# Performance work log

Hardware: AMD Instinct MI355X
Metric: run time of the kernel (lower is better)

Reference implementation:

```python
import jax, jax.numpy as jnp
import numpy as np

N_NODES = 100000
N_EDGES = 1000000
HIDDEN = 128
GROUPS = [[0, 1, 2], [3, 4, 5], [6, 7, 8]]  # model_ids[i]['volume_ids']
COMBOS = [(0, 0), (0, 1), (0, 2), (1, 1), (1, 2), (2, 2)]  # combinations with replacement
LN_EPS = 1e-5


def _ln(h, g, b):
    m = jnp.mean(h, axis=-1, keepdims=True)
    v = jnp.var(h, axis=-1, keepdims=True)
    return (h - m) * jax.lax.rsqrt(v + LN_EPS) * g + b


def setup_inputs() -> dict:
    key = jax.random.key(0)
    ks = jax.random.split(key, 8)
    C = len(COMBOS)
    s = 0.02
    x = jax.random.normal(ks[0], (N_NODES, HIDDEN), jnp.float32)
    e = jax.random.normal(ks[1], (N_EDGES, HIDDEN), jnp.float32)
    edge_index = jax.random.randint(ks[2], (2, N_EDGES), 0, N_NODES)
    volume_id = jax.random.randint(ks[3], (N_NODES,), 0, 9)
    W1 = (jax.random.normal(ks[4], (C, 3 * HIDDEN, HIDDEN), jnp.float32) * s)
    b1 = jnp.zeros((C, HIDDEN), jnp.float32)
    g1 = jnp.ones((C, HIDDEN), jnp.float32)
    be1 = jnp.zeros((C, HIDDEN), jnp.float32)
    W2 = (jax.random.normal(ks[5], (C, HIDDEN, HIDDEN), jnp.float32) * s)
    b2 = jnp.zeros((C, HIDDEN), jnp.float32)
    g2 = jnp.ones((C, HIDDEN), jnp.float32)
    be2 = jnp.zeros((C, HIDDEN), jnp.float32)
    W3 = (jax.random.normal(ks[6], (C, HIDDEN, 1), jnp.float32) * s)
    b3 = jnp.zeros((C, 1), jnp.float32)
    return dict(x=x, edge_index=edge_index, e=e, volume_id=volume_id,
                W1=W1, b1=b1, g1=g1, be1=be1,
                W2=W2, b2=b2, g2=g2, be2=be2,
                W3=W3, b3=b3)


def reference(x, edge_index, e, volume_id, W1, b1, g1, be1, W2, b2, g2, be2, W3, b3):
    # volume id -> group id lookup (constant, from hparams['model_ids'])
    group_of_vol = np.zeros(9, dtype=np.int32)
    for gi, vols in enumerate(GROUPS):
        group_of_vol[vols] = gi
    group_of_vol = jnp.asarray(group_of_vol)

    start, end = edge_index[0], edge_index[1]
    gs = group_of_vol[volume_id[start]]  # [E] group of start node
    ge = group_of_vol[volume_id[end]]    # [E] group of end node
    xs = x[start]                        # [E, H] gather
    xe = x[end]                          # [E, H] gather

    out = jnp.zeros((start.shape[0], 1), x.dtype)
    for c, (ga, gb) in enumerate(COMBOS):
        mask = (gs == ga) & (ge == gb)   # torch.isin on disjoint volume groups
        # split first Linear to avoid materializing concat([xs, xe, e])
        h = xs @ W1[c, :HIDDEN] + xe @ W1[c, HIDDEN:2 * HIDDEN] + e @ W1[c, 2 * HIDDEN:] + b1[c]
        h = jax.nn.relu(_ln(h, g1[c], be1[c]))
        h = jax.nn.relu(_ln(h @ W2[c] + b2[c], g2[c], be2[c]))
        logit = h @ W3[c] + b3[c]        # [E, 1]
        out = jnp.where(mask[:, None], logit, out)  # masked scatter into shared buffer
    return out
```

## Files before the change

### kernel.cpp

```cpp
#include <hip/hip_runtime.h>

#define E_EDGES 1000000
#define N_NODES 100000
#define HID 128

static constexpr int    WS_CMB  = 256;
static constexpr int    WS_LIST = 1000448;
static constexpr int    WS_W1F  = 5001984;
static constexpr int    WS_W2F  = 5591808;

typedef __bf16 bf16x8 __attribute__((ext_vector_type(8)));
typedef float  f32x4  __attribute__((ext_vector_type(4)));

__device__ __forceinline__ unsigned short f2bf(float f) {
    unsigned int u = __builtin_bit_cast(unsigned int, f);
    u = (u + 0x7FFFu + ((u >> 16) & 1u)) >> 16;
    return (unsigned short)u;
}

__global__ void k_wconv(const float* __restrict__ W1, const float* __restrict__ W2,
                        unsigned short* __restrict__ w1f, unsigned short* __restrict__ w2f) {
    int idx = blockIdx.x * 256 + threadIdx.x;
    if (idx < 294912) {
        int j = idx & 7, lane = (idx >> 3) & 63, nt = (idx >> 9) & 7;
        int t = idx >> 12;
        int c = t / 12, kt = t - c * 12;
        int k = kt * 32 + ((lane >> 4) << 3) + j;
        int n = (nt << 4) + (lane & 15);
        w1f[idx] = f2bf(W1[(c * 384 + k) * 128 + n]);
    } else {
        int i2 = idx - 294912;
        int j = i2 & 7, lane = (i2 >> 3) & 63, nt = (i2 >> 9) & 7;
        int t = i2 >> 12;
        int c = t >> 2, kt = t & 3;
        int k = kt * 32 + ((lane >> 4) << 3) + j;
        int n = (nt << 4) + (lane & 15);
        w2f[i2] = f2bf(W2[(c * 128 + k) * 128 + n]);
    }
}

__global__ void k_classify(const int* __restrict__ ei, const int* __restrict__ vol,
                           signed char* __restrict__ cmb, float* __restrict__ out,
                           int* __restrict__ counts) {
    __shared__ int bc[6];
    int tid = threadIdx.x;
    if (tid < 6) bc[tid] = 0;
    __syncthreads();
    int eid = blockIdx.x * 256 + tid;
    if (eid < E_EDGES) {
        int s = ei[eid], t = ei[E_EDGES + eid];
        int gs = vol[s] / 3, ge = vol[t] / 3;
        int cc = -1;
        if (gs <= ge) cc = (gs == 0 ? 0 : (gs == 1 ? 2 : 3)) + ge;
        cmb[eid] = (signed char)cc;
        if (cc < 0) out[eid] = 0.f;
        else atomicAdd(&bc[cc], 1);
    }
    __syncthreads();
    if (tid < 6 && bc[tid] > 0) atomicAdd(&counts[tid], bc[tid]);
}

__global__ void k_offsets(int* __restrict__ ws) {
    if (threadIdx.x == 0 && blockIdx.x == 0) {
        int* counts = ws;
        int* seg    = ws + 16;
        int* tile   = ws + 24;
        int acc = 0;
        for (int c = 0; c < 6; ++c) {
            seg[c]  = acc;
            tile[c] = acc >> 6;
            acc += ((counts[c] + 63) >> 6) << 6;
        }
        seg[6]  = acc;
        tile[6] = acc >> 6;
    }
}

__global__ void k_scatter(const signed char* __restrict__ cmb, int* __restrict__ list,
                          const int* __restrict__ seg, int* __restrict__ cursor) {
    __shared__ int bc[6], basep[6];
    int tid = threadIdx.x;
    if (tid < 6) bc[tid] = 0;
    __syncthreads();
    int eid = blockIdx.x * 256 + tid;
    int cc = -1, lp = 0;
    if (eid < E_EDGES) {
        cc = cmb[eid];
        if (cc >= 0) lp = atomicAdd(&bc[cc], 1);
    }
    __syncthreads();
    if (tid < 6) basep[tid] = bc[tid] > 0 ? atomicAdd(&cursor[tid], bc[tid]) : 0;
    __syncthreads();
    if (cc >= 0) list[seg[cc] + basep[cc] + lp] = eid;
}

__global__ __launch_bounds__(256) void k_mlp(
    const float* __restrict__ x, const int* __restrict__ ei, const float* __restrict__ efeat,
    const int* __restrict__ tile_tab, const int* __restrict__ list,
    const unsigned short* __restrict__ w1f, const unsigned short* __restrict__ w2f,
    const float* __restrict__ b1, const float* __restrict__ g1, const float* __restrict__ be1,
    const float* __restrict__ b2, const float* __restrict__ g2, const float* __restrict__ be2,
    const float* __restrict__ W3, const float* __restrict__ b3,
    float* __restrict__ out)
{
    __shared__ unsigned short H1[4 * 16 * 136];

    int b = blockIdx.x;
    if (b >= tile_tab[6]) return;
    int c = 0;
#pragma unroll
    for (int k = 1; k < 6; ++k) if (b >= tile_tab[k]) c = k;
    int tb = b - tile_tab[c];
    int segbase = tile_tab[c] * 64;

    int tid  = threadIdx.x;
    int lane = tid & 63;
    int wv   = tid >> 6;
    int colb = lane & 15;
    int quad = lane >> 4;

    int eid  = list[segbase + tb * 64 + wv * 16 + colb];
    int eidS = eid >= 0 ? eid : 0;
    int s = ei[eidS], t = ei[E_EDGES + eidS];

    const float* xs = x + (long)s * 128;
    const float* xe = x + (long)t * 128;
    const float* ee = efeat + (long)eidS * 128;

    const bf16x8* w1v = (const bf16x8*)w1f;
    const bf16x8* w2v = (const bf16x8*)w2f;
    const f32x4 zero4 = {0.f, 0.f, 0.f, 0.f};

    f32x4 acc[8];
#pragma unroll
    for (int nt = 0; nt < 8; ++nt) acc[nt] = zero4;
    int koff = quad * 8;
#pragma unroll
    for (int kt = 0; kt < 12; ++kt) {
        const float* src = (kt < 4) ? xs : ((kt < 8) ? xe : ee);
        int o = (kt & 3) * 32 + koff;
        float4 v0 = *(const float4*)(src + o);
        float4 v1 = *(const float4*)(src + o + 4);
        bf16x8 af;
        af[0] = (__bf16)v0.x; af[1] = (__bf16)v0.y; af[2] = (__bf16)v0.z; af[3] = (__bf16)v0.w;
        af[4] = (__bf16)v1.x; af[5] = (__bf16)v1.y; af[6] = (__bf16)v1.z; af[7] = (__bf16)v1.w;
        int wbase = ((c * 12 + kt) * 8) * 64 + lane;
#pragma unroll
        for (int nt = 0; nt < 8; ++nt) {
            bf16x8 bfr = w1v[wbase + nt * 64];
            acc[nt] = __builtin_amdgcn_mfma_f32_16x16x32_bf16(af, bfr, acc[nt], 0, 0, 0);
        }
    }

    float pb[8], pg[8], pe[8];
#pragma unroll
    for (int nt = 0; nt < 8; ++nt) {
        int col = c * 128 + colb + nt * 16;
        pb[nt] = b1[col]; pg[nt] = g1[col]; pe[nt] = be1[col];
    }
    float sum[4] = {0, 0, 0, 0}, sq[4] = {0, 0, 0, 0};
#pragma unroll
    for (int nt = 0; nt < 8; ++nt)
#pragma unroll
        for (int r = 0; r < 4; ++r) {
            float v = acc[nt][r] + pb[nt];
            acc[nt][r] = v;
            sum[r] += v; sq[r] += v * v;
        }
#pragma unroll
    for (int m = 1; m < 16; m <<= 1)
#pragma unroll
        for (int r = 0; r < 4; ++r) {
            sum[r] += __shfl_xor(sum[r], m);
            sq[r]  += __shfl_xor(sq[r], m);
        }
    float mean_[4], rstd_[4];
#pragma unroll
    for (int r = 0; r < 4; ++r) {
        float mu = sum[r] * 0.0078125f;
        float var = sq[r] * 0.0078125f - mu * mu;
        mean_[r] = mu;
        rstd_[r] = rsqrtf(var + 1e-5f);
    }
    int h1base = wv * 2176;
#pragma unroll
    for (int nt = 0; nt < 8; ++nt)
#pragma unroll
        for (int r = 0; r < 4; ++r) {
            float v = (acc[nt][r] - mean_[r]) * rstd_[r] * pg[nt] + pe[nt];
            v = fmaxf(v, 0.f);
            H1[h1base + (quad * 4 + r) * 136 + colb + nt * 16] =
                __builtin_bit_cast(unsigned short, (__bf16)v);
        }

    f32x4 acc2[8];
#pragma unroll
    for (int nt = 0; nt < 8; ++nt) acc2[nt] = zero4;
    int h1row = wv * 2176 + colb * 136 + quad * 8;
#pragma unroll
    for (int kt = 0; kt < 4; ++kt) {
        bf16x8 af = *(const bf16x8*)(&H1[h1row + kt * 32]);
        int wbase = ((c * 4 + kt) * 8) * 64 + lane;
#pragma unroll
        for (int nt = 0; nt < 8; ++nt) {
            bf16x8 bfr = w2v[wbase + nt * 64];
            acc2[nt] = __builtin_amdgcn_mfma_f32_16x16x32_bf16(af, bfr, acc2[nt], 0, 0, 0);
        }
    }

#pragma unroll
    for (int nt = 0; nt < 8; ++nt) {
        int col = c * 128 + colb + nt * 16;
        pb[nt] = b2[col]; pg[nt] = g2[col]; pe[nt] = be2[col];
    }
#pragma unroll
    for (int r = 0; r < 4; ++r) { sum[r] = 0.f; sq[r] = 0.f; }
#pragma unroll
    for (int nt = 0; nt < 8; ++nt)
#pragma unroll
        for (int r = 0; r < 4; ++r) {
            float v = acc2[nt][r] + pb[nt];
            acc2[nt][r] = v;
            sum[r] += v; sq[r] += v * v;
        }
#pragma unroll
    for (int m = 1; m < 16; m <<= 1)
#pragma unroll
        for (int r = 0; r < 4; ++r) {
            sum[r] += __shfl_xor(sum[r], m);
            sq[r]  += __shfl_xor(sq[r], m);
        }
#pragma unroll
    for (int r = 0; r < 4; ++r) {
        float mu = sum[r] * 0.0078125f;
        float var = sq[r] * 0.0078125f - mu * mu;
        mean_[r] = mu;
        rstd_[r] = rsqrtf(var + 1e-5f);
    }
    float w3v[8];
#pragma unroll
    for (int nt = 0; nt < 8; ++nt) w3v[nt] = W3[c * 128 + colb + nt * 16];
    float part[4] = {0, 0, 0, 0};
#pragma unroll
    for (int nt = 0; nt < 8; ++nt)
#pragma unroll
        for (int r = 0; r < 4; ++r) {
            float v = (acc2[nt][r] - mean_[r]) * rstd_[r] * pg[nt] + pe[nt];
            v = fmaxf(v, 0.f);
            part[r] += v * w3v[nt];
        }
#pragma unroll
    for (int m = 1; m < 16; m <<= 1)
#pragma unroll
        for (int r = 0; r < 4; ++r) part[r] += __shfl_xor(part[r], m);

    float b3v = b3[c];
#pragma unroll
    for (int r = 0; r < 4; ++r) {
        int esel = __shfl(eid, quad * 4 + r);
        if (colb == 0 && esel >= 0) out[esel] = part[r] + b3v;
    }
}

extern "C" void kernel_launch(void* const* d_in, const int* in_sizes, int n_in,
                              void* d_out, int out_size, void* d_ws, size_t ws_size,
                              hipStream_t stream) {
    const float* x    = (const float*)d_in[0];
    const int*   ei   = (const int*)d_in[1];
    const float* e    = (const float*)d_in[2];
    const int*   vol  = (const int*)d_in[3];
    const float* W1   = (const float*)d_in[4];
    const float* b1   = (const float*)d_in[5];
    const float* g1   = (const float*)d_in[6];
    const float* be1  = (const float*)d_in[7];
    const float* W2   = (const float*)d_in[8];
    const float* b2   = (const float*)d_in[9];
    const float* g2   = (const float*)d_in[10];
    const float* be2  = (const float*)d_in[11];
    const float* W3   = (const float*)d_in[12];
    const float* b3   = (const float*)d_in[13];
    float* out = (float*)d_out;
    char* wsb = (char*)d_ws;

    hipMemsetAsync(wsb, 0, 256, stream);
    hipMemsetAsync(wsb + WS_LIST, 0xFF, (E_EDGES + 384) * sizeof(int), stream);

    k_wconv<<<1536, 256, 0, stream>>>(W1, W2,
        (unsigned short*)(wsb + WS_W1F), (unsigned short*)(wsb + WS_W2F));
    k_classify<<<(E_EDGES + 255) / 256, 256, 0, stream>>>(ei, vol,
        (signed char*)(wsb + WS_CMB), out, (int*)wsb);
    k_offsets<<<1, 64, 0, stream>>>((int*)wsb);
    k_scatter<<<(E_EDGES + 255) / 256, 256, 0, stream>>>(
        (const signed char*)(wsb + WS_CMB), (int*)(wsb + WS_LIST),
        (const int*)(wsb + 64), (int*)(wsb + 32));
    k_mlp<<<E_EDGES / 64 + 6, 256, 0, stream>>>(
        x, ei, e, (const int*)(wsb + 96), (const int*)(wsb + WS_LIST),
        (const unsigned short*)(wsb + WS_W1F), (const unsigned short*)(wsb + WS_W2F),
        b1, g1, be1, b2, g2, be2, W3, b3, out);
}
```

Before: 1.069 ms.

## Process 32 edges per wave to share weight fragments; spread bin atomics

Each wave in the MLP kernel now runs two 16-edge MFMA tiles against the same weight fragments. This halves the W1/W2 fragment loads from L2 per edge and doubles the gather loads in flight per wave. The per-combination count and cursor atomics are split across 32 slots indexed by block, and a parallel offsets kernel turns them into absolute list positions. This reduces contention on six global counters. The cost is doubled accumulator register pressure (launch bounds now request 4 blocks per SM), which may limit occupancy or cause spills.

New measurement: 1.050 ms. Within noise of the previous version (-1.8%).

```diff
diff --git a/kernel.cpp b/kernel.cpp
--- a/kernel.cpp
+++ b/kernel.cpp
@@ -4,10 +4,10 @@
 #define N_NODES 100000
 #define HID 128
 
-static constexpr int    WS_CMB  = 256;
-static constexpr int    WS_LIST = 1000448;
-static constexpr int    WS_W1F  = 5001984;
-static constexpr int    WS_W2F  = 5591808;
+static constexpr int    WS_CMB  = 1600;
+static constexpr int    WS_LIST = 1001664;
+static constexpr int    WS_W1F  = 5003264;
+static constexpr int    WS_W2F  = 5593088;
 
 typedef __bf16 bf16x8 __attribute__((ext_vector_type(8)));
 typedef float  f32x4  __attribute__((ext_vector_type(4)));
@@ -41,7 +41,7 @@
 
 __global__ void k_classify(const int* __restrict__ ei, const int* __restrict__ vol,
                            signed char* __restrict__ cmb, float* __restrict__ out,
-                           int* __restrict__ counts) {
+                           int* __restrict__ counts2D) {
     __shared__ int bc[6];
     int tid = threadIdx.x;
     if (tid < 6) bc[tid] = 0;
@@ -57,27 +57,32 @@
         else atomicAdd(&bc[cc], 1);
     }
     __syncthreads();
-    if (tid < 6 && bc[tid] > 0) atomicAdd(&counts[tid], bc[tid]);
+    if (tid < 6 && bc[tid] > 0)
+        atomicAdd(&counts2D[tid * 32 + (blockIdx.x & 31)], bc[tid]);
 }
 
 __global__ void k_offsets(int* __restrict__ ws) {
-    if (threadIdx.x == 0 && blockIdx.x == 0) {
-        int* counts = ws;
-        int* seg    = ws + 16;
-        int* tile   = ws + 24;
+    __shared__ int cnt[192], base[192], segs[8];
+    int tid = threadIdx.x;
+    if (tid < 192) cnt[tid] = ws[16 + tid];
+    __syncthreads();
+    if (tid == 0) {
         int acc = 0;
         for (int c = 0; c < 6; ++c) {
-            seg[c]  = acc;
-            tile[c] = acc >> 6;
-            acc += ((counts[c] + 63) >> 6) << 6;
-        }
-        seg[6]  = acc;
-        tile[6] = acc >> 6;
-    }
+            segs[c] = acc;
+            int tot = 0;
+            for (int s = 0; s < 32; ++s) { base[c * 32 + s] = acc + tot; tot += cnt[c * 32 + s]; }
+            acc += ((tot + 63) >> 6) << 6;
+        }
+        segs[6] = acc; segs[7] = 0;
+    }
+    __syncthreads();
+    if (tid < 192) ws[208 + tid] = base[tid];
+    if (tid < 8)   ws[tid] = segs[tid];
 }
 
 __global__ void k_scatter(const signed char* __restrict__ cmb, int* __restrict__ list,
-                          const int* __restrict__ seg, int* __restrict__ cursor) {
+                          int* __restrict__ cursor2D) {
     __shared__ int bc[6], basep[6];
     int tid = threadIdx.x;
     if (tid < 6) bc[tid] = 0;
@@ -89,66 +94,77 @@
         if (cc >= 0) lp = atomicAdd(&bc[cc], 1);
     }
     __syncthreads();
-    if (tid < 6) basep[tid] = bc[tid] > 0 ? atomicAdd(&cursor[tid], bc[tid]) : 0;
-    __syncthreads();
-    if (cc >= 0) list[seg[cc] + basep[cc] + lp] = eid;
-}
-
-__global__ __launch_bounds__(256) void k_mlp(
+    if (tid < 6) basep[tid] = bc[tid] > 0
+        ? atomicAdd(&cursor2D[tid * 32 + (blockIdx.x & 31)], bc[tid]) : 0;
+    __syncthreads();
+    if (cc >= 0) list[basep[cc] + lp] = eid;
+}
+
+__global__ __launch_bounds__(256, 4) void k_mlp(
     const float* __restrict__ x, const int* __restrict__ ei, const float* __restrict__ efeat,
-    const int* __restrict__ tile_tab, const int* __restrict__ list,
+    const int* __restrict__ seg, const int* __restrict__ list,
     const unsigned short* __restrict__ w1f, const unsigned short* __restrict__ w2f,
     const float* __restrict__ b1, const float* __restrict__ g1, const float* __restrict__ be1,
     const float* __restrict__ b2, const float* __restrict__ g2, const float* __restrict__ be2,
     const float* __restrict__ W3, const float* __restrict__ b3,
     float* __restrict__ out)
 {
-    __shared__ unsigned short H1[4 * 16 * 136];
-
-    int b = blockIdx.x;
-    if (b >= tile_tab[6]) return;
-    int c = 0;
-#pragma unroll
-    for (int k = 1; k < 6; ++k) if (b >= tile_tab[k]) c = k;
-    int tb = b - tile_tab[c];
-    int segbase = tile_tab[c] * 64;
+    __shared__ unsigned short H1[4 * 32 * 136];
 
     int tid  = threadIdx.x;
     int lane = tid & 63;
     int wv   = tid >> 6;
+    int p    = blockIdx.x * 128 + wv * 32;
+    if (p >= seg[6]) return;
+    int c = 0;
+#pragma unroll
+    for (int k = 1; k < 6; ++k) if (p >= seg[k]) c = k;
+
     int colb = lane & 15;
     int quad = lane >> 4;
 
-    int eid  = list[segbase + tb * 64 + wv * 16 + colb];
-    int eidS = eid >= 0 ? eid : 0;
-    int s = ei[eidS], t = ei[E_EDGES + eidS];
-
-    const float* xs = x + (long)s * 128;
-    const float* xe = x + (long)t * 128;
-    const float* ee = efeat + (long)eidS * 128;
+    int eid0 = list[p + colb];
+    int eid1 = list[p + 16 + colb];
+    int e0S = eid0 >= 0 ? eid0 : 0;
+    int e1S = eid1 >= 0 ? eid1 : 0;
+    int s0 = ei[e0S], t0 = ei[E_EDGES + e0S];
+    int s1 = ei[e1S], t1 = ei[E_EDGES + e1S];
+
+    const float* xs0 = x + (long)s0 * 128;
+    const float* xe0 = x + (long)t0 * 128;
+    const float* ee0 = efeat + (long)e0S * 128;
+    const float* xs1 = x + (long)s1 * 128;
+    const float* xe1 = x + (long)t1 * 128;
+    const float* ee1 = efeat + (long)e1S * 128;
 
     const bf16x8* w1v = (const bf16x8*)w1f;
     const bf16x8* w2v = (const bf16x8*)w2f;
     const f32x4 zero4 = {0.f, 0.f, 0.f, 0.f};
 
-    f32x4 acc[8];
-#pragma unroll
-    for (int nt = 0; nt < 8; ++nt) acc[nt] = zero4;
+    f32x4 acc0[8], acc1[8];
+#pragma unroll
+    for (int nt = 0; nt < 8; ++nt) { acc0[nt] = zero4; acc1[nt] = zero4; }
     int koff = quad * 8;
 #pragma unroll
     for (int kt = 0; kt < 12; ++kt) {
-        const float* src = (kt < 4) ? xs : ((kt < 8) ? xe : ee);
+        const float* p0 = (kt < 4) ? xs0 : ((kt < 8) ? xe0 : ee0);
+        const float* p1 = (kt < 4) ? xs1 : ((kt < 8) ? xe1 : ee1);
         int o = (kt & 3) * 32 + koff;
-        float4 v0 = *(const float4*)(src + o);
-        float4 v1 = *(const float4*)(src + o + 4);
-        bf16x8 af;
-        af[0] = (__bf16)v0.x; af[1] = (__bf16)v0.y; af[2] = (__bf16)v0.z; af[3] = (__bf16)v0.w;
-        af[4] = (__bf16)v1.x; af[5] = (__bf16)v1.y; af[6] = (__bf16)v1.z; af[7] = (__bf16)v1.w;
-        int wbase = ((c * 12 + kt) * 8) * 64 + lane;
+        float4 va0 = *(const float4*)(p0 + o);
+        float4 va1 = *(const float4*)(p0 + o + 4);
+        float4 vb0 = *(const float4*)(p1 + o);
+        float4 vb1 = *(const float4*)(p1 + o + 4);
+        bf16x8 af0, af1;
+        af0[0] = (__bf16)va0.x; af0[1] = (__bf16)va0.y; af0[2] = (__bf16)va0.z; af0[3] = (__bf16)va0.w;
+        af0[4] = (__bf16)va1.x; af0[5] = (__bf16)va1.y; af0[6] = (__bf16)va1.z; af0[7] = (__bf16)va1.w;
+        af1[0] = (__bf16)vb0.x; af1[1] = (__bf16)vb0.y; af1[2] = (__bf16)vb0.z; af1[3] = (__bf16)vb0.w;
+        af1[4] = (__bf16)vb1.x; af1[5] = (__bf16)vb1.y; af1[6] = (__bf16)vb1.z; af1[7] = (__bf16)vb1.w;
+        int wb = ((c * 12 + kt) * 8) * 64 + lane;
 #pragma unroll
         for (int nt = 0; nt < 8; ++nt) {
-            bf16x8 bfr = w1v[wbase + nt * 64];
-            acc[nt] = __builtin_amdgcn_mfma_f32_16x16x32_bf16(af, bfr, acc[nt], 0, 0, 0);
+            bf16x8 bfr = w1v[wb + nt * 64];
+            acc0[nt] = __builtin_amdgcn_mfma_f32_16x16x32_bf16(af0, bfr, acc0[nt], 0, 0, 0);
+            acc1[nt] = __builtin_amdgcn_mfma_f32_16x16x32_bf16(af1, bfr, acc1[nt], 0, 0, 0);
         }
     }
 
@@ -158,53 +174,60 @@
         int col = c * 128 + colb + nt * 16;
         pb[nt] = b1[col]; pg[nt] = g1[col]; pe[nt] = be1[col];
     }
-    float sum[4] = {0, 0, 0, 0}, sq[4] = {0, 0, 0, 0};
+    float s0a[4] = {0,0,0,0}, q0a[4] = {0,0,0,0}, s1a[4] = {0,0,0,0}, q1a[4] = {0,0,0,0};
 #pragma unroll
     for (int nt = 0; nt < 8; ++nt)
 #pragma unroll
         for (int r = 0; r < 4; ++r) {
-            float v = acc[nt][r] + pb[nt];
-            acc[nt][r] = v;
-            sum[r] += v; sq[r] += v * v;
+            float v = acc0[nt][r] + pb[nt];
+            acc0[nt][r] = v; s0a[r] += v; q0a[r] += v * v;
+            float w = acc1[nt][r] + pb[nt];
+            acc1[nt][r] = w; s1a[r] += w; q1a[r] += w * w;
         }
 #pragma unroll
     for (int m = 1; m < 16; m <<= 1)
 #pragma unroll
         for (int r = 0; r < 4; ++r) {
-            sum[r] += __shfl_xor(sum[r], m);
-            sq[r]  += __shfl_xor(sq[r], m);
-        }
-    float mean_[4], rstd_[4];
+            s0a[r] += __shfl_xor(s0a[r], m); q0a[r] += __shfl_xor(q0a[r], m);
+            s1a[r] += __shfl_xor(s1a[r], m); q1a[r] += __shfl_xor(q1a[r], m);
+        }
+    float mean0[4], rstd0[4], mean1[4], rstd1[4];
 #pragma unroll
     for (int r = 0; r < 4; ++r) {
-        float mu = sum[r] * 0.0078125f;
-        float var = sq[r] * 0.0078125f - mu * mu;
-        mean_[r] = mu;
-        rstd_[r] = rsqrtf(var + 1e-5f);
-    }
-    int h1base = wv * 2176;
+        float mu0 = s0a[r] * 0.0078125f, mu1 = s1a[r] * 0.0078125f;
+        mean0[r] = mu0; rstd0[r] = rsqrtf(q0a[r] * 0.0078125f - mu0 * mu0 + 1e-5f);
+        mean1[r] = mu1; rstd1[r] = rsqrtf(q1a[r] * 0.0078125f - mu1 * mu1 + 1e-5f);
+    }
+    int h1base = wv * 4352;
 #pragma unroll
     for (int nt = 0; nt < 8; ++nt)
 #pragma unroll
         for (int r = 0; r < 4; ++r) {
-            float v = (acc[nt][r] - mean_[r]) * rstd_[r] * pg[nt] + pe[nt];
+            float v = (acc0[nt][r] - mean0[r]) * rstd0[r] * pg[nt] + pe[nt];
             v = fmaxf(v, 0.f);
             H1[h1base + (quad * 4 + r) * 136 + colb + nt * 16] =
                 __builtin_bit_cast(unsigned short, (__bf16)v);
-        }
-
-    f32x4 acc2[8];
-#pragma unroll
-    for (int nt = 0; nt < 8; ++nt) acc2[nt] = zero4;
-    int h1row = wv * 2176 + colb * 136 + quad * 8;
+            float w = (acc1[nt][r] - mean1[r]) * rstd1[r] * pg[nt] + pe[nt];
+            w = fmaxf(w, 0.f);
+            H1[h1base + (16 + quad * 4 + r) * 136 + colb + nt * 16] =
+                __builtin_bit_cast(unsigned short, (__bf16)w);
+        }
+
+    f32x4 acc20[8], acc21[8];
+#pragma unroll
+    for (int nt = 0; nt < 8; ++nt) { acc20[nt] = zero4; acc21[nt] = zero4; }
+    int h1r0 = h1base + colb * 136 + quad * 8;
+    int h1r1 = h1r0 + 16 * 136;
 #pragma unroll
     for (int kt = 0; kt < 4; ++kt) {
-        bf16x8 af = *(const bf16x8*)(&H1[h1row + kt * 32]);
-        int wbase = ((c * 4 + kt) * 8) * 64 + lane;
+        bf16x8 af0 = *(const bf16x8*)(&H1[h1r0 + kt * 32]);
+        bf16x8 af1 = *(const bf16x8*)(&H1[h1r1 + kt * 32]);
+        int wb = ((c * 4 + kt) * 8) * 64 + lane;
 #pragma unroll
         for (int nt = 0; nt < 8; ++nt) {
-            bf16x8 bfr = w2v[wbase + nt * 64];
-            acc2[nt] = __builtin_amdgcn_mfma_f32_16x16x32_bf16(af, bfr, acc2[nt], 0, 0, 0);
+            bf16x8 bfr = w2v[wb + nt * 64];
+            acc20[nt] = __builtin_amdgcn_mfma_f32_16x16x32_bf16(af0, bfr, acc20[nt], 0, 0, 0);
+            acc21[nt] = __builtin_amdgcn_mfma_f32_16x16x32_bf16(af1, bfr, acc21[nt], 0, 0, 0);
         }
     }
 
@@ -214,51 +237,57 @@
         pb[nt] = b2[col]; pg[nt] = g2[col]; pe[nt] = be2[col];
     }
 #pragma unroll
-    for (int r = 0; r < 4; ++r) { sum[r] = 0.f; sq[r] = 0.f; }
+    for (int r = 0; r < 4; ++r) { s0a[r] = 0.f; q0a[r] = 0.f; s1a[r] = 0.f; q1a[r] = 0.f; }
 #pragma unroll
     for (int nt = 0; nt < 8; ++nt)
 #pragma unroll
         for (int r = 0; r < 4; ++r) {
-            float v = acc2[nt][r] + pb[nt];
-            acc2[nt][r] = v;
-            sum[r] += v; sq[r] += v * v;
+            float v = acc20[nt][r] + pb[nt];
+            acc20[nt][r] = v; s0a[r] += v; q0a[r] += v * v;
+            float w = acc21[nt][r] + pb[nt];
+            acc21[nt][r] = w; s1a[r] += w; q1a[r] += w * w;
         }
 #pragma unroll
     for (int m = 1; m < 16; m <<= 1)
 #pragma unroll
         for (int r = 0; r < 4; ++r) {
-            sum[r] += __shfl_xor(sum[r], m);
-            sq[r]  += __shfl_xor(sq[r], m);
+            s0a[r] += __shfl_xor(s0a[r], m); q0a[r] += __shfl_xor(q0a[r], m);
+            s1a[r] += __shfl_xor(s1a[r], m); q1a[r] += __shfl_xor(q1a[r], m);
         }
 #pragma unroll
     for (int r = 0; r < 4; ++r) {
-        float mu = sum[r] * 0.0078125f;
-        float var = sq[r] * 0.0078125f - mu * mu;
-        mean_[r] = mu;
-        rstd_[r] = rsqrtf(var + 1e-5f);
+        float mu0 = s0a[r] * 0.0078125f, mu1 = s1a[r] * 0.0078125f;
+        mean0[r] = mu0; rstd0[r] = rsqrtf(q0a[r] * 0.0078125f - mu0 * mu0 + 1e-5f);
+        mean1[r] = mu1; rstd1[r] = rsqrtf(q1a[r] * 0.0078125f - mu1 * mu1 + 1e-5f);
     }
     float w3v[8];
 #pragma unroll
     for (int nt = 0; nt < 8; ++nt) w3v[nt] = W3[c * 128 + colb + nt * 16];
-    float part[4] = {0, 0, 0, 0};
+    float part0[4] = {0,0,0,0}, part1[4] = {0,0,0,0};
 #pragma unroll
     for (int nt = 0; nt < 8; ++nt)
 #pragma unroll
         for (int r = 0; r < 4; ++r) {
-            float v = (acc2[nt][r] - mean_[r]) * rstd_[r] * pg[nt] + pe[nt];
-            v = fmaxf(v, 0.f);
-            part[r] += v * w3v[nt];
+            float v = (acc20[nt][r] - mean0[r]) * rstd0[r] * pg[nt] + pe[nt];
+            part0[r] += fmaxf(v, 0.f) * w3v[nt];
+            float w = (acc21[nt][r] - mean1[r]) * rstd1[r] * pg[nt] + pe[nt];
+            part1[r] += fmaxf(w, 0.f) * w3v[nt];
         }
 #pragma unroll
     for (int m = 1; m < 16; m <<= 1)
 #pragma unroll
-        for (int r = 0; r < 4; ++r) part[r] += __shfl_xor(part[r], m);
+        for (int r = 0; r < 4; ++r) {
+            part0[r] += __shfl_xor(part0[r], m);
+            part1[r] += __shfl_xor(part1[r], m);
+        }
 
     float b3v = b3[c];
 #pragma unroll
     for (int r = 0; r < 4; ++r) {
-        int esel = __shfl(eid, quad * 4 + r);
-        if (colb == 0 && esel >= 0) out[esel] = part[r] + b3v;
+        int es0 = __shfl(eid0, quad * 4 + r);
+        int es1 = __shfl(eid1, quad * 4 + r);
+        if (colb == 0 && es0 >= 0) out[es0] = part0[r] + b3v;
+        if (colb == 0 && es1 >= 0) out[es1] = part1[r] + b3v;
     }
 }
 
@@ -282,19 +311,19 @@
     float* out = (float*)d_out;
     char* wsb = (char*)d_ws;
 
-    hipMemsetAsync(wsb, 0, 256, stream);
+    hipMemsetAsync(wsb, 0, 1600, stream);
     hipMemsetAsync(wsb + WS_LIST, 0xFF, (E_EDGES + 384) * sizeof(int), stream);
 
     k_wconv<<<1536, 256, 0, stream>>>(W1, W2,
         (unsigned short*)(wsb + WS_W1F), (unsigned short*)(wsb + WS_W2F));
     k_classify<<<(E_EDGES + 255) / 256, 256, 0, stream>>>(ei, vol,
-        (signed char*)(wsb + WS_CMB), out, (int*)wsb);
-    k_offsets<<<1, 64, 0, stream>>>((int*)wsb);
+        (signed char*)(wsb + WS_CMB), out, (int*)(wsb + 64));
+    k_offsets<<<1, 256, 0, stream>>>((int*)wsb);
     k_scatter<<<(E_EDGES + 255) / 256, 256, 0, stream>>>(
         (const signed char*)(wsb + WS_CMB), (int*)(wsb + WS_LIST),
-        (const int*)(wsb + 64), (int*)(wsb + 32));
-    k_mlp<<<E_EDGES / 64 + 6, 256, 0, stream>>>(
-        x, ei, e, (const int*)(wsb + 96), (const int*)(wsb + WS_LIST),
+        (int*)(wsb + 832));
+    k_mlp<<<E_EDGES / 128 + 6, 256, 0, stream>>>(
+        x, ei, e, (const int*)wsb, (const int*)(wsb + WS_LIST),
         (const unsigned short*)(wsb + WS_W1F), (const unsigned short*)(wsb + WS_W2F),
         b1, g1, be1, b2, g2, be2, W3, b3, out);
 }
```
